# Optimization experiments

Hardware: AMD Instinct MI355X
Metric: run time of the kernel (lower is better)

## Reference

```python
import jax, jax.numpy as jnp
import numpy as np

EMBED_DIMS = 128
NUM_HEADS = 4
NUM_LAYERS = 3
OUT_CHANNELS = 20
PROJECT_SCALE = 4
VOXEL_SIZE = 0.2
SCENE_FULL = (256, 256, 32)
SCENE = tuple(s // PROJECT_SCALE for s in SCENE_FULL)  # (64, 64, 8)
NQ = SCENE[0] * SCENE[1] * SCENE[2]                    # 32768
N_INST = 100
NUM_CLS = 21
IMAGE_SHAPE = (48, 160)
ORI_IMAGE_SHAPE = (384, 1280)
SCORE_THR, MASK_THR, IOU_THR = 0.25, 0.5, 0.8
DILATIONS = (1, 2, 3)


def _generate_grid(grid_shape, value):
    axes = [np.linspace(0, v - 1, s, dtype=np.float32) for s, v in zip(grid_shape, value)]
    return np.stack(np.meshgrid(*axes, indexing='ij'), 0)


def _layer_norm(x, g, b):
    mu = x.mean(-1, keepdims=True)
    var = ((x - mu) ** 2).mean(-1, keepdims=True)
    return (x - mu) * jax.lax.rsqrt(var + 1e-5) * g + b


def _mha(q, k, v, bias, in_w, in_b, out_w, out_b):
    C = q.shape[-1]
    H, D = NUM_HEADS, q.shape[-1] // NUM_HEADS
    wq, wk, wv = jnp.split(in_w, 3, axis=0)
    bq, bk, bv = jnp.split(in_b, 3)
    qh = (q @ wq.T + bq).reshape(q.shape[0], q.shape[1], H, D)
    kh = (k @ wk.T + bk).reshape(k.shape[0], k.shape[1], H, D)
    vh = (v @ wv.T + bv).reshape(v.shape[0], v.shape[1], H, D)
    s = jnp.einsum('bqhd,bkhd->bhqk', qh, kh) * (1.0 / np.sqrt(D)) + bias
    a = jax.nn.softmax(s, axis=-1)
    o = jnp.einsum('bhqk,bkhd->bqhd', a, vh).reshape(q.shape)
    return o @ out_w.T + out_b


def _conv3d(x, w, b, dilation):
    pad = (w.shape[-1] // 2) * dilation
    y = jax.lax.conv_general_dilated(
        x, w, window_strides=(1, 1, 1), padding=[(pad, pad)] * 3,
        rhs_dilation=(dilation,) * 3,
        dimension_numbers=('NCDHW', 'OIDHW', 'NCDHW'))
    return y + b[None, :, None, None, None]


def _forward(inst_queries, pred_logits, pred_masks, depth, K, E, voxel_origin,
             query_embed_w, pos_embed_w, attn_in_w, attn_in_b, attn_out_w,
             attn_out_b, ln1_g, ln1_b, ffn_w1, ffn_b1, ffn_w2, ffn_b2,
             ln2_g, ln2_b, proc_w, proc_b, out_w, out_b, fov_mask):
    C = EMBED_DIMS
    h, w = IMAGE_SHAPE
    n = pred_masks.shape[1]
    # buffers (compile-time constants)
    image_grid = jnp.asarray(_generate_grid(IMAGE_SHAPE, ORI_IMAGE_SHAPE)[::-1].copy())  # [2,h,w] (x,y)
    qp = (_generate_grid(SCENE, SCENE) + 0.5) * VOXEL_SIZE * PROJECT_SCALE
    query_pos0 = jnp.asarray(qp.reshape(3, -1).T)[None]  # [1,NQ,3]

    # panoptic postprocess (masked form, bs=1; invalid instance slots masked, not dropped)
    probs = jax.nn.softmax(jax.nn.sigmoid(pred_logits) / 0.06, axis=-1)
    scores = probs.max(-1)[0]              # [n]; labels.ne(num_classes) always True
    keep0 = scores > SCORE_THR
    pm = jax.nn.sigmoid(pred_masks[0])     # [n,h,w]
    prob_masks = jnp.where(keep0[:, None, None], scores[:, None, None] * pm, -1.0)
    mask_ids = jnp.argmax(prob_masks, axis=0)   # [h,w]
    masks = (mask_ids[None] == jnp.arange(n)[:, None, None]) & keep0[:, None, None]
    mask_area = masks.reshape(n, -1).sum(-1).astype(jnp.float32)
    pm_bin = pm >= MASK_THR
    pm_area = pm_bin.reshape(n, -1).sum(-1).astype(jnp.float32)
    masks = masks & pm_bin
    inter = masks.reshape(n, -1).sum(-1)
    keep = keep0 & (inter > 0) & (mask_area >= IOU_THR * pm_area)
    masks = masks & keep[:, None, None]
    any_keep = keep.any()

    # gather_mask_pos: back-project masked pixels to 3D and sum per instance
    d = depth.reshape(1, 1, h, w)
    grid = jnp.concatenate([image_grid[None] * d, d], axis=1).reshape(1, 3, h * w)
    cam = jnp.linalg.inv(K) @ grid
    hom = jnp.concatenate([cam, jnp.ones((1, 1, h * w), cam.dtype)], axis=1)
    pts = (jnp.linalg.inv(E) @ hom)[0, :3].T       # [HW,3]
    inst_xyz = masks.reshape(n, -1).astype(pts.dtype) @ pts  # [n,3] gather-mask-sum
    inst_pos = (inst_xyz @ pos_embed_w.T)[None]    # [1,n,C]

    # cross-attention over all scene queries; fov gather/scatter folded into final where,
    # valid because per-query computation is independent in cross-attn + per-token FFN/LN.
    qpos = (query_pos0 + voxel_origin) @ pos_embed_w.T        # [1,NQ,C]
    use = jnp.where(any_keep, 1.0, 0.0).astype(inst_queries.dtype)
    kv_k = inst_queries + use * inst_pos
    key_mask = jnp.where(any_keep, keep, True)
    bias = jnp.where(key_mask, 0.0, -1e9)[None, None, None, :]  # [1,1,1,n]
    q = query_embed_w[None]
    for li in range(NUM_LAYERS):
        x = q + qpos
        a = _mha(x, kv_k, inst_queries, bias, attn_in_w[li], attn_in_b[li],
                 attn_out_w[li], attn_out_b[li])
        x = _layer_norm(a + x, ln1_g[li], ln1_b[li])
        f = jax.nn.gelu(x @ ffn_w1[li].T + ffn_b1[li], approximate=False) @ ffn_w2[li].T + ffn_b2[li]
        q = _layer_norm(f + x, ln2_g[li], ln2_b[li])

    q = jnp.where(fov_mask[..., None], q, query_embed_w[None])   # scatter-update query_embed_src[fov_mask]
    x3d = q.reshape(1, *SCENE, C).transpose(0, 4, 1, 2, 3)       # [1,C,X,Y,Z]
    for i, dil in enumerate(DILATIONS):                          # Process: dilated residual convs
        x3d = jax.nn.relu(_conv3d(x3d, proc_w[i], proc_b[i], dil) + x3d)
    return _conv3d(x3d, out_w, out_b, 1)                         # [1,out_ch,X,Y,Z]


def setup_inputs():
    key = jax.random.key(0)
    ks = jax.random.split(key, 16)
    C, L = EMBED_DIMS, NUM_LAYERS
    s = 0.02
    inp = {}
    inp['inst_queries'] = jax.random.normal(ks[0], (1, N_INST, C), jnp.float32)
    inp['pred_logits'] = jax.random.normal(ks[1], (1, N_INST, NUM_CLS), jnp.float32)
    inp['pred_masks'] = jax.random.normal(ks[2], (1, N_INST) + IMAGE_SHAPE, jnp.float32) * 2.0
    inp['depth'] = jax.random.uniform(ks[3], (1,) + IMAGE_SHAPE, jnp.float32, 1.0, 50.0)
    inp['K'] = jnp.array([[[500.0, 0.0, 640.0], [0.0, 500.0, 192.0], [0.0, 0.0, 1.0]]], jnp.float32)
    inp['E'] = jnp.eye(4, dtype=jnp.float32).at[:3, 3].set(jnp.array([0.5, -0.3, 1.2]))[None]
    inp['voxel_origin'] = jax.random.normal(ks[4], (1, 1, 3), jnp.float32)
    inp['query_embed_w'] = jax.random.normal(ks[5], (NQ, C), jnp.float32) * s
    inp['pos_embed_w'] = jax.random.normal(ks[6], (C, 3), jnp.float32) * 2e-4
    inp['attn_in_w'] = jax.random.normal(ks[7], (L, 3 * C, C), jnp.float32) * s
    inp['attn_in_b'] = jnp.zeros((L, 3 * C), jnp.float32)
    inp['attn_out_w'] = jax.random.normal(ks[8], (L, C, C), jnp.float32) * s
    inp['attn_out_b'] = jnp.zeros((L, C), jnp.float32)
    inp['ln1_g'] = jnp.ones((L, C), jnp.float32)
    inp['ln1_b'] = jnp.zeros((L, C), jnp.float32)
    inp['ffn_w1'] = jax.random.normal(ks[9], (L, 4 * C, C), jnp.float32) * s
    inp['ffn_b1'] = jnp.zeros((L, 4 * C), jnp.float32)
    inp['ffn_w2'] = jax.random.normal(ks[10], (L, C, 4 * C), jnp.float32) * s
    inp['ffn_b2'] = jnp.zeros((L, C), jnp.float32)
    inp['ln2_g'] = jnp.ones((L, C), jnp.float32)
    inp['ln2_b'] = jnp.zeros((L, C), jnp.float32)
    inp['proc_w'] = jax.random.normal(ks[11], (3, C, C, 3, 3, 3), jnp.float32) * s
    inp['proc_b'] = jnp.zeros((3, C), jnp.float32)
    inp['out_w'] = jax.random.normal(ks[12], (OUT_CHANNELS, C, 1, 1, 1), jnp.float32) * s
    inp['out_b'] = jnp.zeros((OUT_CHANNELS,), jnp.float32)
    inp['fov_mask'] = jax.random.bernoulli(ks[13], 0.5, (1, NQ))
    return inp


def reference(inst_queries, pred_logits, pred_masks, depth, K, E, voxel_origin,
              query_embed_w, pos_embed_w, attn_in_w, attn_in_b, attn_out_w,
              attn_out_b, ln1_g, ln1_b, ffn_w1, ffn_b1, ffn_w2, ffn_b2,
              ln2_g, ln2_b, proc_w, proc_b, out_w, out_b, fov_mask):
    return _forward(inst_queries, pred_logits, pred_masks, depth, K, E, voxel_origin,
                    query_embed_w, pos_embed_w, attn_in_w, attn_in_b, attn_out_w,
                    attn_out_b, ln1_g, ln1_b, ffn_w1, ffn_b1, ffn_w2, ffn_b2,
                    ln2_g, ln2_b, proc_w, proc_b, out_w, out_b, fov_mask)
```

## Files before the change

### kernel.cpp

```cpp
#include <hip/hip_runtime.h>
#include <math.h>

typedef unsigned short u16;
typedef unsigned int   u32;

#define NQv 32768
#define HWp 7680
#define NI  100

typedef short v8s __attribute__((ext_vector_type(8)));
typedef float v4f __attribute__((ext_vector_type(4)));

__device__ inline float bf2f(u16 u){ u32 x = ((u32)u) << 16; return __uint_as_float(x); }
__device__ inline u16 f2bf(float f){
  u32 x = __float_as_uint(f);
  u32 r = (x + 0x7fffu + ((x >> 16) & 1u)) >> 16;
  return (u16)r;
}
__device__ inline float sigf(float x){ return 1.0f / (1.0f + expf(-x)); }

typedef const __attribute__((address_space(1))) void* gas_t;
typedef __attribute__((address_space(3))) void* las_t;

__global__ void k_prep_small(const float* __restrict__ Km, const float* __restrict__ Em,
                             const float* __restrict__ logits,
                             float* __restrict__ mats, float* __restrict__ scores,
                             int* __restrict__ keep0)
{
  int tid = threadIdx.x;
  if (tid == 0) {
    double a[9];
    for (int i = 0; i < 9; i++) a[i] = (double)Km[i];
    double det = a[0]*(a[4]*a[8]-a[5]*a[7]) - a[1]*(a[3]*a[8]-a[5]*a[6]) + a[2]*(a[3]*a[7]-a[4]*a[6]);
    double id = 1.0 / det;
    double inv[9];
    inv[0]=(a[4]*a[8]-a[5]*a[7])*id; inv[1]=(a[2]*a[7]-a[1]*a[8])*id; inv[2]=(a[1]*a[5]-a[2]*a[4])*id;
    inv[3]=(a[5]*a[6]-a[3]*a[8])*id; inv[4]=(a[0]*a[8]-a[2]*a[6])*id; inv[5]=(a[2]*a[3]-a[0]*a[5])*id;
    inv[6]=(a[3]*a[7]-a[4]*a[6])*id; inv[7]=(a[1]*a[6]-a[0]*a[7])*id; inv[8]=(a[0]*a[4]-a[1]*a[3])*id;
    for (int i = 0; i < 9; i++) mats[i] = (float)inv[i];
    double m[4][8];
    for (int r = 0; r < 4; r++){
      for (int c = 0; c < 4; c++){ m[r][c] = (double)Em[r*4+c]; m[r][4+c] = (r==c) ? 1.0 : 0.0; }
    }
    for (int col = 0; col < 4; col++){
      int piv = col; double best = fabs(m[col][col]);
      for (int r = col+1; r < 4; r++){ double v = fabs(m[r][col]); if (v > best){ best = v; piv = r; } }
      if (piv != col){ for (int c = 0; c < 8; c++){ double t = m[col][c]; m[col][c] = m[piv][c]; m[piv][c] = t; } }
      double p = m[col][col];
      for (int c = 0; c < 8; c++) m[col][c] /= p;
      for (int r = 0; r < 4; r++) if (r != col){ double f = m[r][col]; for (int c = 0; c < 8; c++) m[r][c] -= f*m[col][c]; }
    }
    for (int r = 0; r < 3; r++) for (int c = 0; c < 4; c++) mats[9 + r*4 + c] = (float)m[r][4+c];
  }
  if (tid < NI) {
    float mx = -1e30f;
    for (int c = 0; c < 21; c++){ float t = sigf(logits[tid*21+c]) / 0.06f; mx = fmaxf(mx, t); }
    float s = 0.f;
    for (int c = 0; c < 21; c++){ float t = sigf(logits[tid*21+c]) / 0.06f; s += expf(t - mx); }
    float sc = 1.0f / s;
    scores[tid] = sc;
    keep0[tid] = (sc > 0.25f) ? 1 : 0;
  }
}

__global__ void k_prep_multi(
    const float* __restrict__ s0, u16* __restrict__ d0, int n0,
    const float* __restrict__ s1, u16* __restrict__ d1, int n1,
    const float* __restrict__ s2, u16* __restrict__ d2, int n2,
    const float* __restrict__ s3, u16* __restrict__ d3, int n3,
    u16* __restrict__ z0, int zn0, u16* __restrict__ z1, int zn1,
    u16* __restrict__ z2, int zn2,
    const float* __restrict__ pe, float* __restrict__ peT)
{
  int i = blockIdx.x*256 + threadIdx.x;
  if (i < n0){ d0[i] = f2bf(s0[i]); return; } i -= n0;
  if (i < n1){ d1[i] = f2bf(s1[i]); return; } i -= n1;
  if (i < n2){ d2[i] = f2bf(s2[i]); return; } i -= n2;
  if (i < n3){ d3[i] = f2bf(s3[i]); return; } i -= n3;
  if (i < zn0){ z0[i] = 0; return; } i -= zn0;
  if (i < zn1){ z1[i] = 0; return; } i -= zn1;
  if (i < zn2){ z2[i] = 0; return; } i -= zn2;
  if (i < 384){ int d = i >> 7, c = i & 127; peT[i] = pe[c*3 + d]; }
}

__global__ __launch_bounds__(256) void k_mask_argmax2(
    const float* __restrict__ pmL, const float* __restrict__ scores,
    const int* __restrict__ keep0, int* __restrict__ mids)
{
  __shared__ float sv[4][64];
  __shared__ int   si[4][64];
  int tid = threadIdx.x, lane = tid & 63, w = tid >> 6;
  int p = blockIdx.x*64 + lane;
  float best = -2e30f; int bid = 0;
  #pragma unroll 5
  for (int jj = 0; jj < 25; jj++){
    int i = w*25 + jj;
    float lg = pmL[i*HWp + p];
    float val = keep0[i] ? scores[i] * sigf(lg) : -1.0f;
    if (val > best){ best = val; bid = i; }
  }
  sv[w][lane] = best; si[w][lane] = bid;
  __syncthreads();
  if (w == 0){
    float b0 = sv[0][lane]; int i0 = si[0][lane];
    #pragma unroll
    for (int g = 1; g < 4; g++){
      float bg = sv[g][lane]; int ig = si[g][lane];
      if (bg > b0 || (bg == b0 && ig < i0)){ b0 = bg; i0 = ig; }
    }
    mids[p] = i0;
  }
}

__global__ __launch_bounds__(256) void k_instbp(
    const float* __restrict__ pmL, const int* __restrict__ mids,
    const int* __restrict__ keep0, const float* __restrict__ depth,
    const float* __restrict__ mats, int* __restrict__ keep, float* __restrict__ xyz)
{
  int i = blockIdx.x, tid = threadIdx.x;
  int k0 = keep0[i];
  int ma = 0, pa = 0, it = 0;
  for (int p = tid; p < HWp; p += 256){
    float lg = pmL[i*HWp + p];
    int pb = (lg >= 0.0f) ? 1 : 0;
    int mi = (mids[p] == i && k0) ? 1 : 0;
    ma += mi; pa += pb; it += (mi & pb);
  }
  __shared__ int sma[256], spa[256], sit[256];
  __shared__ int s_keep;
  sma[tid] = ma; spa[tid] = pa; sit[tid] = it;
  __syncthreads();
  for (int off = 128; off; off >>= 1){
    if (tid < off){ sma[tid]+=sma[tid+off]; spa[tid]+=spa[tid+off]; sit[tid]+=sit[tid+off]; }
    __syncthreads();
  }
  if (tid == 0){
    int kk = (k0 && sit[0] > 0 && ((float)sma[0] >= 0.8f*(float)spa[0])) ? 1 : 0;
    keep[i] = kk; s_keep = kk;
  }
  __syncthreads();
  float sx = 0.f, sy = 0.f, sz = 0.f;
  if (s_keep){
    float ik0=mats[0],ik1=mats[1],ik2=mats[2],ik3=mats[3],ik4=mats[4],ik5=mats[5],ik6=mats[6],ik7=mats[7],ik8=mats[8];
    const float* iE = mats + 9;
    for (int p = tid; p < HWp; p += 256){
      if (mids[p] == i && pmL[i*HWp + p] >= 0.0f){
        int r = p / 160, c = p % 160;
        float xg = (float)((double)c * (1279.0/159.0));
        float yg = (float)((double)r * (383.0/47.0));
        float d = depth[p];
        float g0 = xg*d, g1 = yg*d, g2 = d;
        float c0 = ik0*g0 + ik1*g1 + ik2*g2;
        float c1 = ik3*g0 + ik4*g1 + ik5*g2;
        float c2 = ik6*g0 + ik7*g1 + ik8*g2;
        sx += iE[0]*c0 + iE[1]*c1 + iE[2]*c2 + iE[3];
        sy += iE[4]*c0 + iE[5]*c1 + iE[6]*c2 + iE[7];
        sz += iE[8]*c0 + iE[9]*c1 + iE[10]*c2 + iE[11];
      }
    }
  }
  __shared__ float rx[256], ry[256], rz[256];
  rx[tid]=sx; ry[tid]=sy; rz[tid]=sz;
  __syncthreads();
  for (int off = 128; off; off >>= 1){
    if (tid < off){ rx[tid]+=rx[tid+off]; ry[tid]+=ry[tid+off]; rz[tid]+=rz[tid+off]; }
    __syncthreads();
  }
  if (tid == 0){ xyz[i*3+0]=rx[0]; xyz[i*3+1]=ry[0]; xyz[i*3+2]=rz[0]; }
}

__global__ void k_kvk(const float* __restrict__ iq, const float* __restrict__ pe,
                      const float* __restrict__ xyz, const int* __restrict__ keep,
                      float* __restrict__ kvk)
{
  int tid = threadIdx.x;
  unsigned long long b = __ballot(tid < 100 && keep[tid] != 0);
  __shared__ int s_w[4];
  if ((tid & 63) == 0) s_w[tid >> 6] = (b != 0ULL);
  __syncthreads();
  float u = (s_w[0] | s_w[1]) ? 1.0f : 0.0f;
  int idx = blockIdx.x*256 + tid;
  if (idx >= NI*128) return;
  int i = idx >> 7, c = idx & 127;
  float ip = pe[c*3+0]*xyz[i*3+0] + pe[c*3+1]*xyz[i*3+1] + pe[c*3+2]*xyz[i*3+2];
  kvk[idx] = iq[idx] + u * ip;
}

__global__ __launch_bounds__(512) void k_khvh2(const float* __restrict__ kvk,
    const float* __restrict__ iq, const float* __restrict__ Win,
    const float* __restrict__ bin, const int* __restrict__ keep,
    float* __restrict__ biasArr, u16* __restrict__ khs_bf, u16* __restrict__ vt_bf)
{
  __shared__ u16 s_in[NI][130];
  __shared__ u16 s_w[64][130];
  __shared__ int s_any[8];
  int li = blockIdx.x, c0 = blockIdx.y*64;
  bool isK = (c0 < 128);
  const float* srcIn = isK ? kvk : iq;
  int tid = threadIdx.x;
  unsigned long long bm = __ballot(tid < 100 && keep[tid] != 0);
  if ((tid & 63) == 0) s_any[tid >> 6] = (bm != 0ULL);
  for (int i = tid; i < NI*128; i += 512) s_in[i>>7][i&127] = f2bf(srcIn[i]);
  const float* wbase = Win + ((size_t)li*384 + 128 + c0)*128;
  for (int i = tid; i < 64*128; i += 512) s_w[i>>7][i&127] = f2bf(wbase[i]);
  __syncthreads();
  if (li == 0 && c0 == 0 && tid < 128){
    int any = s_any[0] | s_any[1];
    float bb;
    if (tid < NI) bb = any ? (keep[tid] ? 0.0f : -1e9f) : 0.0f;
    else bb = -1e9f;
    biasArr[tid] = bb;
  }
  for (int o = tid; o < NI*64; o += 512){
    int k = o >> 6, c = o & 63;
    float acc = 0.f;
    #pragma unroll 8
    for (int j = 0; j < 128; j++) acc += bf2f(s_in[k][j]) * bf2f(s_w[c][j]);
    int cc = c0 + c;
    float v = acc + bin[li*384 + 128 + cc];
    int ch = cc & 127;
    int h = ch >> 5, dim = ch & 31;
    size_t hb = ((size_t)li*4 + h)*4096;
    if (isK){
      int kt = k >> 4, c16 = k & 15, r4q = dim >> 3, d = dim & 7;
      khs_bf[hb + kt*512 + (r4q*16 + c16)*8 + d] = f2bf(v * 0.17677669529663687f);
    } else {
      int dt = dim >> 4, c16d = dim & 15, ks = k >> 5, r4k = (k >> 3) & 3, d = k & 7;
      vt_bf[hb + (ks*2 + dt)*512 + (r4k*16 + c16d)*8 + d] = f2bf(v);
    }
  }
}

__global__ __launch_bounds__(256) void k_packconv2(const float* __restrict__ w, u16* __restrict__ wp)
{
  __shared__ u16 s[3456];
  int o = blockIdx.x, li = blockIdx.y;
  const float* src = w + ((size_t)li*128 + o)*3456;
  for (int t = threadIdx.x; t < 3456; t += 256) s[t] = f2bf(src[t]);
  __syncthreads();
  for (int e = threadIdx.x; e < 3456; e += 256){
    int t = e >> 7, i = e & 127;
    wp[(((size_t)li*27 + t)*128 + o)*128 + i] = s[i*27 + t];
  }
}

__device__ inline void stage128(const u16* __restrict__ G, u16* lds,
                                int rbase, int pitchK, int kofs)
{
  int lane = threadIdx.x & 63, w = threadIdx.x >> 6;
  #pragma unroll
  for (int s = 0; s < 4; s++){
    int ldsOff = s*8192 + w*1024 + lane*16;
    int row = ldsOff >> 8;
    int cb  = ldsOff & 255;
    int scb = cb ^ ((row & 7) << 4);
    const u16* src = G + (size_t)(rbase + row)*pitchK + kofs + (scb >> 1);
    u16* dst = lds + (s*4096 + w*512);
    __builtin_amdgcn_global_load_lds((gas_t)src, (las_t)dst, 16, 0, 0);
  }
}

__device__ inline void copy32k(const u16* __restrict__ G, u16* lds)
{
  int lane = threadIdx.x & 63, w = threadIdx.x >> 6;
  #pragma unroll
  for (int s = 0; s < 4; s++){
    int off = s*4096 + w*512;
    const u16* src = G + off + lane*8;
    __builtin_amdgcn_global_load_lds((gas_t)src, (las_t)(lds + off), 16, 0, 0);
  }
}

__device__ inline void stageConvA4(const u16* __restrict__ X, const u16* __restrict__ zp,
                                   u16* lds, int m0, int dx, int dy)
{
  int lane = threadIdx.x & 63, w = threadIdx.x >> 6;
  #pragma unroll
  for (int s = 0; s < 4; s++){
    int ldsOff = s*8192 + w*1024 + lane*16;
    int row = ldsOff >> 8;
    int cb  = ldsOff & 255;
    int scb = cb ^ ((row & 7) << 4);
    int sidx = m0 + row;
    int xs = (sidx >> 9) + dx, ys = ((sidx >> 3) & 63) + dy, zs = sidx & 7;
    bool ok = ((unsigned)xs < 64u) & ((unsigned)ys < 64u);
    const u16* src = ok ? (X + (size_t)((xs*64+ys)*8+zs)*128 + (scb>>1)) : (zp + (scb>>1));
    u16* dst = lds + (s*4096 + w*512);
    __builtin_amdgcn_global_load_lds((gas_t)src, (las_t)dst, 16, 0, 0);
  }
}

__device__ inline v8s fragld(const u16* base, int row, int cb){
  return *(const v8s*)(base + row*128 + (((cb) ^ ((row & 7) << 4)) >> 1));
}

__device__ inline void compute128(const u16* As, const u16* Bs,
                                  int wm, int wn, int r15, int kg, v4f acc[2][4])
{
  #pragma unroll
  for (int k0 = 0; k0 < 4; k0++){
    int cb = k0*64 + kg*16;
    v8s a0 = fragld(As, wm*32 +      r15, cb);
    v8s a1 = fragld(As, wm*32 + 16 + r15, cb);
    v8s b0 = fragld(Bs, wn*64 +      r15, cb);
    v8s b1 = fragld(Bs, wn*64 + 16 + r15, cb);
    v8s b2 = fragld(Bs, wn*64 + 32 + r15, cb);
    v8s b3 = fragld(Bs, wn*64 + 48 + r15, cb);
    acc[0][0] = __builtin_amdgcn_mfma_f32_16x16x32_bf16(a0, b0, acc[0][0], 0, 0, 0);
    acc[0][1] = __builtin_amdgcn_mfma_f32_16x16x32_bf16(a0, b1, acc[0][1], 0, 0, 0);
    acc[0][2] = __builtin_amdgcn_mfma_f32_16x16x32_bf16(a0, b2, acc[0][2], 0, 0, 0);
    acc[0][3] = __builtin_amdgcn_mfma_f32_16x16x32_bf16(a0, b3, acc[0][3], 0, 0, 0);
    acc[1][0] = __builtin_amdgcn_mfma_f32_16x16x32_bf16(a1, b0, acc[1][0], 0, 0, 0);
    acc[1][1] = __builtin_amdgcn_mfma_f32_16x16x32_bf16(a1, b1, acc[1][1], 0, 0, 0);
    acc[1][2] = __builtin_amdgcn_mfma_f32_16x16x32_bf16(a1, b2, acc[1][2], 0, 0, 0);
    acc[1][3] = __builtin_amdgcn_mfma_f32_16x16x32_bf16(a1, b3, acc[1][3], 0, 0, 0);
  }
}

__global__ __launch_bounds__(512) void k_layer(
    const void* __restrict__ srcv, int srcBf,
    const float* __restrict__ peT, const float* __restrict__ vo,
    const u16* __restrict__ ainQ, const float* __restrict__ ainQb,
    const u16* __restrict__ khs, const u16* __restrict__ vt,
    const float* __restrict__ biasArr,
    const u16* __restrict__ aoutw, const float* __restrict__ aoutb,
    const float* __restrict__ g1, const float* __restrict__ b1v,
    const u16* __restrict__ w1p, const float* __restrict__ b1p,
    const u16* __restrict__ w2p, const float* __restrict__ b2p,
    const float* __restrict__ g2, const float* __restrict__ b2v,
    u16* __restrict__ outB, const int* __restrict__ fov, const float* __restrict__ qe)
{
  extern __shared__ u16 smem[];
  u16* SA = smem;
  u16* SB = smem + 16384;
  u16* X  = smem + 32768;
  u16* Rh = smem + 49152;
  char* Xc = (char*)X;
  char* Rc = (char*)Rh;
  int tid = threadIdx.x, lane = tid & 63, w = tid >> 6;
  int wm = w & 3, wn = w >> 2, r15 = lane & 15, kg = lane >> 4;
  int m0 = blockIdx.x * 128;

  stage128(ainQ, SA, 0, 128, 0);
  copy32k(khs, Rh);
  copy32k(vt, Rh + 16384);
  {
    int r = tid >> 2, c0 = (tid & 3)*32;
    int q = m0 + r;
    float px = ((float)(q >> 9)       + 0.5f)*0.8f + vo[0];
    float py = ((float)((q >> 3)&63)  + 0.5f)*0.8f + vo[1];
    float pz = ((float)(q & 7)        + 0.5f)*0.8f + vo[2];
    char* arow = Xc + r*256;
    int rx = (r & 7) << 4;
    if (!srcBf){
      const float4* sp  = (const float4*)((const float*)srcv + (size_t)q*128 + c0);
      const float4* pex = (const float4*)(peT +   0 + c0);
      const float4* pey = (const float4*)(peT + 128 + c0);
      const float4* pez = (const float4*)(peT + 256 + c0);
      #pragma unroll
      for (int j = 0; j < 8; j++){
        float4 v = sp[j];
        float4 ax = pex[j], ay = pey[j], az = pez[j];
        float o0 = v.x + ax.x*px + ay.x*py + az.x*pz;
        float o1 = v.y + ax.y*px + ay.y*py + az.y*pz;
        float o2 = v.z + ax.z*px + ay.z*py + az.z*pz;
        float o3 = v.w + ax.w*px + ay.w*py + az.w*pz;
        int cbyte = (c0 + j*4)*2;
        *(u32*)(arow + ((cbyte    ) ^ rx)) = (u32)f2bf(o0) | ((u32)f2bf(o1) << 16);
        *(u32*)(arow + ((cbyte + 4) ^ rx)) = (u32)f2bf(o2) | ((u32)f2bf(o3) << 16);
      }
    } else {
      const u16* sp = (const u16*)srcv + (size_t)q*128 + c0;
      #pragma unroll
      for (int j = 0; j < 4; j++){
        v8s t = *(const v8s*)(sp + j*8);
        #pragma unroll
        for (int pr = 0; pr < 4; pr++){
          int c = c0 + j*8 + pr*2;
          float e0 = bf2f((u16)t[pr*2])   + peT[c]*px   + peT[128+c]*py   + peT[256+c]*pz;
          float e1 = bf2f((u16)t[pr*2+1]) + peT[c+1]*px + peT[128+c+1]*py + peT[256+c+1]*pz;
          *(u32*)(arow + ((c*2) ^ rx)) = (u32)f2bf(e0) | ((u32)f2bf(e1) << 16);
        }
      }
    }
  }
  __syncthreads();

  {
    v4f acc[2][4] = {};
    compute128(X, SA, wm, wn, r15, kg, acc);
    #pragma unroll
    for (int i = 0; i < 2; i++){
      #pragma unroll
      for (int j = 0; j < 4; j++){
        int col = wn*64 + j*16 + r15;
        float bv = ainQb[col];
        #pragma unroll
        for (int rr = 0; rr < 4; rr++){
          int row = wm*32 + i*16 + kg*4 + rr;
          *(u16*)((char*)SB + row*256 + (((col*2)) ^ ((row & 7) << 4))) = f2bf(acc[i][j][rr] + bv);
        }
      }
    }
  }
  __syncthreads();

  {
    int c = lane & 15, r4 = lane >> 4;
    char* pwc = (char*)(SA + w*2048);
    int qrow_base = w*16;
    #pragma unroll
    for (int h = 0; h < 4; h++){
      const u16* Kh = Rh + h*4096;
      const u16* Vh = Rh + 16384 + h*4096;
      int qrow = qrow_base + c;
      v8s qf = *(const v8s*)((char*)SB + qrow*256 + ((h*64 + r4*16) ^ ((qrow & 7) << 4)));
      v4f s[8] = {{0,0,0,0},{0,0,0,0},{0,0,0,0},{0,0,0,0},{0,0,0,0},{0,0,0,0},{0,0,0,0},{0,0,0,0}};
      #pragma unroll
      for (int kt = 0; kt < 8; kt++){
        v8s kf = *(const v8s*)(Kh + kt*512 + lane*8);
        s[kt] = __builtin_amdgcn_mfma_f32_16x16x32_bf16(kf, qf, s[kt], 0, 0, 0);
      }
      float mx = -1e30f;
      #pragma unroll
      for (int kt = 0; kt < 8; kt++){
        float4 bb = *(const float4*)(biasArr + kt*16 + r4*4);
        s[kt][0] += bb.x; s[kt][1] += bb.y; s[kt][2] += bb.z; s[kt][3] += bb.w;
        mx = fmaxf(mx, fmaxf(fmaxf(s[kt][0], s[kt][1]), fmaxf(s[kt][2], s[kt][3])));
      }
      mx = fmaxf(mx, __shfl_xor(mx, 16, 64));
      mx = fmaxf(mx, __shfl_xor(mx, 32, 64));
      float sum = 0.f;
      #pragma unroll
      for (int kt = 0; kt < 8; kt++){
        #pragma unroll
        for (int rg = 0; rg < 4; rg++){
          float p = __expf(s[kt][rg] - mx);
          s[kt][rg] = p; sum += p;
        }
      }
      sum += __shfl_xor(sum, 16, 64);
      sum += __shfl_xor(sum, 32, 64);
      float inv = 1.0f / sum;
      int rxq = (c & 7) << 4;
      #pragma unroll
      for (int kt = 0; kt < 8; kt++){
        #pragma unroll
        for (int pr = 0; pr < 2; pr++){
          u32 pk = (u32)f2bf(s[kt][pr*2]*inv) | ((u32)f2bf(s[kt][pr*2+1]*inv) << 16);
          int colb = kt*32 + r4*8 + pr*4;
          *(u32*)(pwc + c*256 + (colb ^ rxq)) = pk;
        }
      }
      v4f o[2] = {{0,0,0,0},{0,0,0,0}};
      #pragma unroll
      for (int ks = 0; ks < 4; ks++){
        v8s aP = *(const v8s*)(pwc + c*256 + ((ks*64 + r4*16) ^ rxq));
        #pragma unroll
        for (int dt = 0; dt < 2; dt++){
          v8s vf = *(const v8s*)(Vh + (ks*2 + dt)*512 + lane*8);
          o[dt] = __builtin_amdgcn_mfma_f32_16x16x32_bf16(aP, vf, o[dt], 0, 0, 0);
        }
      }
      #pragma unroll
      for (int dt = 0; dt < 2; dt++){
        #pragma unroll
        for (int rg = 0; rg < 4; rg++){
          int row = qrow_base + r4*4 + rg;
          int col = h*32 + dt*16 + c;
          *(u16*)((char*)SB + row*256 + ((col*2) ^ ((row & 7) << 4))) = f2bf(o[dt][rg]);
        }
      }
    }
  }
  __syncthreads();

  stage128(aoutw, SA, 0, 128, 0);
  __syncthreads();
  {
    v4f acc[2][4] = {};
    compute128(SB, SA, wm, wn, r15, kg, acc);
    #pragma unroll
    for (int i = 0; i < 2; i++){
      #pragma unroll
      for (int j = 0; j < 4; j++){
        int col = wn*64 + j*16 + r15;
        float bv = aoutb[col];
        #pragma unroll
        for (int rr = 0; rr < 4; rr++){
          int row = wm*32 + i*16 + kg*4 + rr;
          float xres = bf2f(*(const u16*)(Xc + row*256 + ((col*2) ^ ((row & 7) << 4))));
          float y = acc[i][j][rr] + bv + xres;
          *(float*)(Rc + row*512 + ((col*4) ^ ((row & 7) << 4))) = y;
        }
      }
    }
  }
  __syncthreads();

  {
    int r = tid >> 2, j4 = tid & 3;
    float vals[32];
    int rx = (r & 7) << 4;
    #pragma unroll
    for (int k = 0; k < 32; k++){
      int c = j4 + 4*k;
      vals[k] = *(const float*)(Rc + r*512 + ((c*4) ^ rx));
    }
    float s = 0.f;
    #pragma unroll
    for (int k = 0; k < 32; k++) s += vals[k];
    s += __shfl_xor(s, 1, 64); s += __shfl_xor(s, 2, 64);
    float mean = s * (1.0f/128.0f);
    float vv = 0.f;
    #pragma unroll
    for (int k = 0; k < 32; k++){ float d = vals[k] - mean; vv += d*d; }
    vv += __shfl_xor(vv, 1, 64); vv += __shfl_xor(vv, 2, 64);
    float rs = rsqrtf(vv*(1.0f/128.0f) + 1e-5f);
    #pragma unroll
    for (int k = 0; k < 32; k++){
      int c = j4 + 4*k;
      float o = (vals[k] - mean)*rs*g1[c] + b1v[c];
      *(float*)(Rc + r*512 + ((c*4) ^ rx)) = o;
      *(u16*)(Xc + r*256 + ((c*2) ^ rx)) = f2bf(o);
    }
  }
  __syncthreads();

  v4f acc2[2][4] = {};
  for (int nt = 0; nt < 4; nt++){
    stage128(w1p, SA, nt*128, 128, 0);
    stage128(w2p, SB, 0, 512, nt*128);
    __syncthreads();
    v4f a1[2][4] = {};
    compute128(X, SA, wm, wn, r15, kg, a1);
    __syncthreads();
    #pragma unroll
    for (int i = 0; i < 2; i++){
      #pragma unroll
      for (int j = 0; j < 4; j++){
        int col = wn*64 + j*16 + r15;
        float bv = b1p[nt*128 + col];
        #pragma unroll
        for (int rr = 0; rr < 4; rr++){
          int row = wm*32 + i*16 + kg*4 + rr;
          float hv = a1[i][j][rr] + bv;
          float u2 = hv*(0.7978845608028654f + 0.0356774081f*hv*hv);
          hv = hv / (1.0f + __expf(-2.0f*u2));
          *(u16*)((char*)SA + row*256 + ((col*2) ^ ((row & 7) << 4))) = f2bf(hv);
        }
      }
    }
    __syncthreads();
    compute128(SA, SB, wm, wn, r15, kg, acc2);
    __syncthreads();
  }

  {
    #pragma unroll
    for (int i = 0; i < 2; i++){
      #pragma unroll
      for (int j = 0; j < 4; j++){
        int col = wn*64 + j*16 + r15;
        float bv = b2p[col];
        #pragma unroll
        for (int rr = 0; rr < 4; rr++){
          int row = wm*32 + i*16 + kg*4 + rr;
          char* p = Rc + row*512 + ((col*4) ^ ((row & 7) << 4));
          float y = acc2[i][j][rr] + bv + *(const float*)p;
          *(float*)p = y;
        }
      }
    }
  }
  __syncthreads();

  {
    int r = tid >> 2, j4 = tid & 3;
    float vals[32];
    int rx = (r & 7) << 4;
    #pragma unroll
    for (int k = 0; k < 32; k++){
      int c = j4 + 4*k;
      vals[k] = *(const float*)(Rc + r*512 + ((c*4) ^ rx));
    }
    float s = 0.f;
    #pragma unroll
    for (int k = 0; k < 32; k++) s += vals[k];
    s += __shfl_xor(s, 1, 64); s += __shfl_xor(s, 2, 64);
    float mean = s * (1.0f/128.0f);
    float vv = 0.f;
    #pragma unroll
    for (int k = 0; k < 32; k++){ float d = vals[k] - mean; vv += d*d; }
    vv += __shfl_xor(vv, 1, 64); vv += __shfl_xor(vv, 2, 64);
    float rs = rsqrtf(vv*(1.0f/128.0f) + 1e-5f);
    int gq = m0 + r;
    #pragma unroll
    for (int k = 0; k < 32; k++){
      int c = j4 + 4*k;
      float o = (vals[k] - mean)*rs*g2[c] + b2v[c];
      if (fov){
        outB[(size_t)gq*128 + c] = f2bf(fov[gq] ? o : qe[(size_t)gq*128 + c]);
      } else {
        outB[(size_t)gq*128 + c] = f2bf(o);
      }
    }
  }
}

__global__ __launch_bounds__(512) void k_conv4(
    const u16* __restrict__ X, const u16* __restrict__ W,
    const float* __restrict__ bias, const u16* __restrict__ zp,
    u16* __restrict__ Y, int dil)
{
  extern __shared__ u16 smem[];
  u16* bufA0 = smem;
  u16* bufA1 = smem + 16384;
  u16* bufW0 = smem + 32768;
  u16* bufW1 = smem + 49152;
  int tid = threadIdx.x, lane = tid & 63, w = tid >> 6;
  int wk = w & 1, wm = (w >> 1) & 1, wn = (w >> 2) & 1;
  int r15 = lane & 15, kg = lane >> 4;
  int bid = blockIdx.x;
  int lb = (bid & 7)*32 + (bid >> 3);
  int m0 = lb*128;
  v4f acc[4][4] = {};
  const v8s vzero = {0,0,0,0,0,0,0,0};
  stageConvA4(X, zp, bufA0, m0, -dil, -dil);
  stage128(W, bufW0, 0, 128, 0);
  for (int g = 0; g < 9; g++){
    const u16* As = (g & 1) ? bufA1 : bufA0;
    #pragma unroll
    for (int dzi = 0; dzi < 3; dzi++){
      int t = g*3 + dzi;
      const u16* Ws = (t & 1) ? bufW1 : bufW0;
      if (t + 1 < 27)
        stage128(W + (size_t)(t+1)*16384, ((t+1)&1) ? bufW1 : bufW0, 0, 128, 0);
      if (dzi == 0 && g < 8){
        int gn = g + 1;
        stageConvA4(X, zp, (gn & 1) ? bufA1 : bufA0, m0, (gn/3 - 1)*dil, (gn%3 - 1)*dil);
      }
      if (dzi == 0){
        if (g < 8) asm volatile("s_waitcnt vmcnt(8)" ::: "memory");
        else       asm volatile("s_waitcnt vmcnt(4)" ::: "memory");
      } else {
        if (t < 26) asm volatile("s_waitcnt vmcnt(4)" ::: "memory");
        else        asm volatile("s_waitcnt vmcnt(0)" ::: "memory");
      }
      __builtin_amdgcn_s_barrier();
      asm volatile("" ::: "memory");
      int zofs = (dzi - 1)*dil;
      bool okz = (unsigned)((r15 & 7) + zofs) < 8u;
      #pragma unroll
      for (int k0 = 0; k0 < 2; k0++){
        int cb = wk*128 + k0*64 + kg*16;
        v8s a[4], b[4];
        #pragma unroll
        for (int q = 0; q < 4; q++){
          int ra = wm*64 + q*16 + r15 + zofs;
          int rc = min(max(ra, 0), 127);
          a[q] = okz ? fragld(As, rc, cb) : vzero;
          b[q] = fragld(Ws, wn*64 + q*16 + r15, cb);
        }
        #pragma unroll
        for (int i = 0; i < 4; i++)
          #pragma unroll
          for (int j = 0; j < 4; j++)
            acc[i][j] = __builtin_amdgcn_mfma_f32_16x16x32_bf16(a[i], b[j], acc[i][j], 0, 0, 0);
      }
      asm volatile("" ::: "memory");
      __builtin_amdgcn_s_barrier();
      asm volatile("" ::: "memory");
    }
  }
  float* red = (float*)smem;
  if (wk == 0){
    #pragma unroll
    for (int i = 0; i < 4; i++)
      #pragma unroll
      for (int j = 0; j < 4; j++)
        #pragma unroll
        for (int rr = 0; rr < 4; rr++)
          red[(wm*64 + i*16 + kg*4 + rr)*128 + wn*64 + j*16 + r15] = acc[i][j][rr];
  }
  __syncthreads();
  if (wk == 1){
    #pragma unroll
    for (int i = 0; i < 4; i++){
      #pragma unroll
      for (int j = 0; j < 4; j++){
        int col = wn*64 + j*16 + r15;
        float bv = bias[col];
        #pragma unroll
        for (int rr = 0; rr < 4; rr++){
          int row = wm*64 + i*16 + kg*4 + rr;
          int grow = m0 + row;
          float v = acc[i][j][rr] + red[row*128 + col] + bv + bf2f(X[(size_t)grow*128 + col]);
          v = fmaxf(v, 0.0f);
          Y[(size_t)grow*128 + col] = f2bf(v);
        }
      }
    }
  }
}

__global__ __launch_bounds__(256) void k_outconv(const u16* __restrict__ X,
    const float* __restrict__ W, const float* __restrict__ B, float* __restrict__ out)
{
  __shared__ float sw[20*128];
  __shared__ float sbb[20];
  int tid = threadIdx.x;
  for (int i = tid; i < 20*128; i += 256) sw[i] = W[i];
  if (tid < 20) sbb[tid] = B[tid];
  __syncthreads();
  int s = blockIdx.x*256 + tid;
  u32 rv[64];
  const u32* xp = (const u32*)(X + (size_t)s*128);
  #pragma unroll
  for (int j = 0; j < 64; j++) rv[j] = xp[j];
  for (int ot = 0; ot < 20; ot++){
    float acc = sbb[ot];
    #pragma unroll
    for (int j = 0; j < 64; j++){
      u32 u = rv[j];
      acc += bf2f((u16)(u & 0xffff))*sw[ot*128 + 2*j] + bf2f((u16)(u >> 16))*sw[ot*128 + 2*j + 1];
    }
    out[(size_t)ot*NQv + s] = acc;
  }
}

extern "C" void kernel_launch(void* const* d_in, const int* in_sizes, int n_in,
                              void* d_out, int out_size, void* d_ws, size_t ws_size,
                              hipStream_t stream)
{
  const float* iq    = (const float*)d_in[0];
  const float* logits= (const float*)d_in[1];
  const float* pmL   = (const float*)d_in[2];
  const float* depth = (const float*)d_in[3];
  const float* Km    = (const float*)d_in[4];
  const float* Em    = (const float*)d_in[5];
  const float* vo    = (const float*)d_in[6];
  const float* qe    = (const float*)d_in[7];
  const float* pe    = (const float*)d_in[8];
  const float* ain_w = (const float*)d_in[9];
  const float* ain_b = (const float*)d_in[10];
  const float* aout_w= (const float*)d_in[11];
  const float* aout_b= (const float*)d_in[12];
  const float* ln1g  = (const float*)d_in[13];
  const float* ln1b  = (const float*)d_in[14];
  const float* w1    = (const float*)d_in[15];
  const float* b1    = (const float*)d_in[16];
  const float* w2    = (const float*)d_in[17];
  const float* b2    = (const float*)d_in[18];
  const float* ln2g  = (const float*)d_in[19];
  const float* ln2b  = (const float*)d_in[20];
  const float* pw    = (const float*)d_in[21];
  const float* pb    = (const float*)d_in[22];
  const float* ow    = (const float*)d_in[23];
  const float* ob    = (const float*)d_in[24];
  const int*   fov   = (const int*)d_in[25];
  float* out = (float*)d_out;

  (void)hipFuncSetAttribute((const void*)k_layer, hipFuncAttributeMaxDynamicSharedMemorySize, 163840);
  (void)hipFuncSetAttribute((const void*)k_conv4, hipFuncAttributeMaxDynamicSharedMemorySize, 131072);

  char* ws = (char*)d_ws;
  size_t off = 0;
  auto alloc = [&](size_t bytes) -> char* {
    char* p = ws + off;
    off = (off + bytes + 255) & ~(size_t)255;
    return p;
  };
  float* mats    = (float*)alloc(32*4);
  float* scores  = (float*)alloc(128*4);
  int*   keep0   = (int*)  alloc(128*4);
  int*   keep    = (int*)  alloc(128*4);
  float* biasArr = (float*)alloc(128*4);
  float* xyz     = (float*)alloc(512*4);
  u16*   zp      = (u16*)  alloc(256);
  float* peT     = (float*)alloc(384*4);
  int*   mids    = (int*)  alloc((size_t)HWp*4);
  float* kvkb    = (float*)alloc((size_t)NI*128*4);
  u16* khs_bf  = (u16*)alloc((size_t)3*4*128*32*2);
  u16* vt_bf   = (u16*)alloc((size_t)3*4*32*128*2);
  u16* ain_bf  = (u16*)alloc((size_t)3*384*128*2);
  u16* aout_bf = (u16*)alloc((size_t)3*128*128*2);
  u16* w1_bf   = (u16*)alloc((size_t)3*512*128*2);
  u16* w2_bf   = (u16*)alloc((size_t)3*128*512*2);
  u16* wc_bf   = (u16*)alloc((size_t)3*27*128*128*2);
  u16* T2bf = (u16*)alloc((size_t)NQv*128*2);
  u16* x3a  = (u16*)alloc((size_t)NQv*128*2);
  u16* x3b  = (u16*)alloc((size_t)NQv*128*2);
  (void)ws_size; (void)in_sizes; (void)n_in; (void)out_size;

  k_prep_small<<<1,128,0,stream>>>(Km, Em, logits, mats, scores, keep0);
  {
    int n0 = 3*384*128, n1 = 3*128*128, n2 = 3*512*128, n3 = 3*128*512;
    int zn0 = 3*4*128*32, zn1 = 3*4*32*128, zn2 = 128;
    int total = n0+n1+n2+n3+zn0+zn1+zn2+384;
    k_prep_multi<<<(total+255)/256,256,0,stream>>>(
        ain_w, ain_bf, n0, aout_w, aout_bf, n1, w1, w1_bf, n2, w2, w2_bf, n3,
        khs_bf, zn0, vt_bf, zn1, zp, zn2, pe, peT);
  }
  k_packconv2<<<dim3(128,3),256,0,stream>>>(pw, wc_bf);
  k_mask_argmax2<<<120,256,0,stream>>>(pmL, scores, keep0, mids);
  k_instbp<<<NI,256,0,stream>>>(pmL, mids, keep0, depth, mats, keep, xyz);
  k_kvk<<<(NI*128+255)/256,256,0,stream>>>(iq, pe, xyz, keep, kvkb);
  { dim3 g(3,4); k_khvh2<<<g,512,0,stream>>>(kvkb, iq, ain_w, ain_b, keep, biasArr, khs_bf, vt_bf); }

  for (int li = 0; li < 3; li++){
    const void* src = (li == 0) ? (const void*)qe : (const void*)T2bf;
    u16* outT = (li < 2) ? T2bf : x3a;
    k_layer<<<256,512,163840,stream>>>(
        src, (li == 0) ? 0 : 1, peT, vo,
        ain_bf + (size_t)li*384*128, ain_b + li*384,
        khs_bf + (size_t)li*16384, vt_bf + (size_t)li*16384, biasArr,
        aout_bf + (size_t)li*128*128, aout_b + li*128,
        ln1g + li*128, ln1b + li*128,
        w1_bf + (size_t)li*512*128, b1 + li*512,
        w2_bf + (size_t)li*128*512, b2 + li*128,
        ln2g + li*128, ln2b + li*128,
        outT, (li == 2) ? fov : nullptr, qe);
  }

  k_conv4<<<256,512,131072,stream>>>(x3a, wc_bf + (size_t)0*27*16384, pb + 0,   zp, x3b, 1);
  k_conv4<<<256,512,131072,stream>>>(x3b, wc_bf + (size_t)1*27*16384, pb + 128, zp, x3a, 2);
  k_conv4<<<256,512,131072,stream>>>(x3a, wc_bf + (size_t)2*27*16384, pb + 256, zp, x3b, 3);
  k_outconv<<<128,256,0,stream>>>(x3b, ow, ob, out);
}
```

Measured before the change: 362.3 us.

## Halve k_layer tile to 64 queries and shrink LDS to fit more blocks

Restructures the fused transformer layer kernel to process 64 query rows per block instead of 128, doubling the grid to 512 blocks. LDS use drops from 160KB to 80KB by reusing three 32KB-class buffers, loading K/V heads in two halves, and keeping residuals in bf16 rather than fp32. The aim is more concurrent blocks per CU and better use of all CUs on the GPU. In exchange it adds extra barriers, restages weight tiles twice as often across blocks, and rounds the FFN residual to bf16, which may change numerics slightly.

```diff
diff --git a/kernel.cpp b/kernel.cpp
--- a/kernel.cpp
+++ b/kernel.cpp
@@ -260,11 +260,11 @@
   }
 }
 
-__device__ inline void copy32k(const u16* __restrict__ G, u16* lds)
+__device__ inline void copy16k(const u16* __restrict__ G, u16* lds)
 {
   int lane = threadIdx.x & 63, w = threadIdx.x >> 6;
   #pragma unroll
-  for (int s = 0; s < 4; s++){
+  for (int s = 0; s < 2; s++){
     int off = s*4096 + w*512;
     const u16* src = G + off + lane*8;
     __builtin_amdgcn_global_load_lds((gas_t)src, (las_t)(lds + off), 16, 0, 0);
@@ -294,30 +294,24 @@
   return *(const v8s*)(base + row*128 + (((cb) ^ ((row & 7) << 4)) >> 1));
 }
 
-__device__ inline void compute128(const u16* As, const u16* Bs,
-                                  int wm, int wn, int r15, int kg, v4f acc[2][4])
+__device__ inline void compute64(const u16* As, const u16* Bs,
+                                 int wm, int wn, int r15, int kg, v4f acc[2][2])
 {
   #pragma unroll
   for (int k0 = 0; k0 < 4; k0++){
     int cb = k0*64 + kg*16;
     v8s a0 = fragld(As, wm*32 +      r15, cb);
     v8s a1 = fragld(As, wm*32 + 16 + r15, cb);
-    v8s b0 = fragld(Bs, wn*64 +      r15, cb);
-    v8s b1 = fragld(Bs, wn*64 + 16 + r15, cb);
-    v8s b2 = fragld(Bs, wn*64 + 32 + r15, cb);
-    v8s b3 = fragld(Bs, wn*64 + 48 + r15, cb);
+    v8s b0 = fragld(Bs, wn*32 +      r15, cb);
+    v8s b1 = fragld(Bs, wn*32 + 16 + r15, cb);
     acc[0][0] = __builtin_amdgcn_mfma_f32_16x16x32_bf16(a0, b0, acc[0][0], 0, 0, 0);
     acc[0][1] = __builtin_amdgcn_mfma_f32_16x16x32_bf16(a0, b1, acc[0][1], 0, 0, 0);
-    acc[0][2] = __builtin_amdgcn_mfma_f32_16x16x32_bf16(a0, b2, acc[0][2], 0, 0, 0);
-    acc[0][3] = __builtin_amdgcn_mfma_f32_16x16x32_bf16(a0, b3, acc[0][3], 0, 0, 0);
     acc[1][0] = __builtin_amdgcn_mfma_f32_16x16x32_bf16(a1, b0, acc[1][0], 0, 0, 0);
     acc[1][1] = __builtin_amdgcn_mfma_f32_16x16x32_bf16(a1, b1, acc[1][1], 0, 0, 0);
-    acc[1][2] = __builtin_amdgcn_mfma_f32_16x16x32_bf16(a1, b2, acc[1][2], 0, 0, 0);
-    acc[1][3] = __builtin_amdgcn_mfma_f32_16x16x32_bf16(a1, b3, acc[1][3], 0, 0, 0);
-  }
-}
-
-__global__ __launch_bounds__(512) void k_layer(
+  }
+}
+
+__global__ __launch_bounds__(512, 4) void k_layer(
     const void* __restrict__ srcv, int srcBf,
     const float* __restrict__ peT, const float* __restrict__ vo,
     const u16* __restrict__ ainQ, const float* __restrict__ ainQb,
@@ -331,48 +325,43 @@
     u16* __restrict__ outB, const int* __restrict__ fov, const float* __restrict__ qe)
 {
   extern __shared__ u16 smem[];
-  u16* SA = smem;
-  u16* SB = smem + 16384;
-  u16* X  = smem + 32768;
-  u16* Rh = smem + 49152;
-  char* Xc = (char*)X;
-  char* Rc = (char*)Rh;
+  u16* A = smem;
+  u16* B = smem + 16384;
+  u16* C = smem + 32768;
+  char* Ac = (char*)A;
+  char* Cc = (char*)C;
   int tid = threadIdx.x, lane = tid & 63, w = tid >> 6;
-  int wm = w & 3, wn = w >> 2, r15 = lane & 15, kg = lane >> 4;
-  int m0 = blockIdx.x * 128;
-
-  stage128(ainQ, SA, 0, 128, 0);
-  copy32k(khs, Rh);
-  copy32k(vt, Rh + 16384);
+  int wm = w & 1, wn = w >> 1, r15 = lane & 15, kg = lane >> 4;
+  int m0 = blockIdx.x * 64;
+
+  stage128(ainQ, A, 0, 128, 0);
+  copy16k(khs, B);
+  copy16k(vt, B + 8192);
   {
-    int r = tid >> 2, c0 = (tid & 3)*32;
+    int r = tid >> 3, c0 = (tid & 7)*16;
     int q = m0 + r;
     float px = ((float)(q >> 9)       + 0.5f)*0.8f + vo[0];
     float py = ((float)((q >> 3)&63)  + 0.5f)*0.8f + vo[1];
     float pz = ((float)(q & 7)        + 0.5f)*0.8f + vo[2];
-    char* arow = Xc + r*256;
+    char* arow = Cc + r*256;
     int rx = (r & 7) << 4;
     if (!srcBf){
       const float4* sp  = (const float4*)((const float*)srcv + (size_t)q*128 + c0);
-      const float4* pex = (const float4*)(peT +   0 + c0);
-      const float4* pey = (const float4*)(peT + 128 + c0);
-      const float4* pez = (const float4*)(peT + 256 + c0);
-      #pragma unroll
-      for (int j = 0; j < 8; j++){
+      #pragma unroll
+      for (int j = 0; j < 4; j++){
         float4 v = sp[j];
-        float4 ax = pex[j], ay = pey[j], az = pez[j];
-        float o0 = v.x + ax.x*px + ay.x*py + az.x*pz;
-        float o1 = v.y + ax.y*px + ay.y*py + az.y*pz;
-        float o2 = v.z + ax.z*px + ay.z*py + az.z*pz;
-        float o3 = v.w + ax.w*px + ay.w*py + az.w*pz;
-        int cbyte = (c0 + j*4)*2;
-        *(u32*)(arow + ((cbyte    ) ^ rx)) = (u32)f2bf(o0) | ((u32)f2bf(o1) << 16);
-        *(u32*)(arow + ((cbyte + 4) ^ rx)) = (u32)f2bf(o2) | ((u32)f2bf(o3) << 16);
+        int c = c0 + j*4;
+        float o0 = v.x + peT[c]*px   + peT[128+c]*py   + peT[256+c]*pz;
+        float o1 = v.y + peT[c+1]*px + peT[128+c+1]*py + peT[256+c+1]*pz;
+        float o2 = v.z + peT[c+2]*px + peT[128+c+2]*py + peT[256+c+2]*pz;
+        float o3 = v.w + peT[c+3]*px + peT[128+c+3]*py + peT[256+c+3]*pz;
+        *(u32*)(arow + ((c*2    ) ^ rx)) = (u32)f2bf(o0) | ((u32)f2bf(o1) << 16);
+        *(u32*)(arow + ((c*2 + 4) ^ rx)) = (u32)f2bf(o2) | ((u32)f2bf(o3) << 16);
       }
     } else {
       const u16* sp = (const u16*)srcv + (size_t)q*128 + c0;
       #pragma unroll
-      for (int j = 0; j < 4; j++){
+      for (int j = 0; j < 2; j++){
         v8s t = *(const v8s*)(sp + j*8);
         #pragma unroll
         for (int pr = 0; pr < 4; pr++){
@@ -387,18 +376,19 @@
   __syncthreads();
 
   {
-    v4f acc[2][4] = {};
-    compute128(X, SA, wm, wn, r15, kg, acc);
+    v4f acc[2][2] = {};
+    compute64(C, A, wm, wn, r15, kg, acc);
+    __syncthreads();
     #pragma unroll
     for (int i = 0; i < 2; i++){
       #pragma unroll
-      for (int j = 0; j < 4; j++){
-        int col = wn*64 + j*16 + r15;
+      for (int j = 0; j < 2; j++){
+        int col = wn*32 + j*16 + r15;
         float bv = ainQb[col];
         #pragma unroll
         for (int rr = 0; rr < 4; rr++){
           int row = wm*32 + i*16 + kg*4 + rr;
-          *(u16*)((char*)SB + row*256 + (((col*2)) ^ ((row & 7) << 4))) = f2bf(acc[i][j][rr] + bv);
+          *(u16*)(Ac + row*256 + ((col*2) ^ ((row & 7) << 4))) = f2bf(acc[i][j][rr] + bv);
         }
       }
     }
@@ -407,19 +397,32 @@
 
   {
     int c = lane & 15, r4 = lane >> 4;
-    char* pwc = (char*)(SA + w*2048);
-    int qrow_base = w*16;
-    #pragma unroll
-    for (int h = 0; h < 4; h++){
-      const u16* Kh = Rh + h*4096;
-      const u16* Vh = Rh + 16384 + h*4096;
-      int qrow = qrow_base + c;
-      v8s qf = *(const v8s*)((char*)SB + qrow*256 + ((h*64 + r4*16) ^ ((qrow & 7) << 4)));
+    int qt = w & 3, hsel = w >> 2;
+    int qrow = qt*16 + c;
+    v8s qf[2];
+    #pragma unroll
+    for (int p = 0; p < 2; p++){
+      int h = p*2 + hsel;
+      qf[p] = *(const v8s*)(Ac + qrow*256 + ((h*64 + r4*16) ^ ((qrow & 7) << 4)));
+    }
+    __syncthreads();
+    char* pwc = (char*)(A + w*2048);
+    v4f out[2][2];
+    #pragma unroll
+    for (int p = 0; p < 2; p++){
+      if (p == 1){
+        __syncthreads();
+        copy16k(khs + 8192, B);
+        copy16k(vt + 8192, B + 8192);
+        __syncthreads();
+      }
+      const u16* Kh = B + hsel*4096;
+      const u16* Vh = B + 8192 + hsel*4096;
       v4f s[8] = {{0,0,0,0},{0,0,0,0},{0,0,0,0},{0,0,0,0},{0,0,0,0},{0,0,0,0},{0,0,0,0},{0,0,0,0}};
       #pragma unroll
       for (int kt = 0; kt < 8; kt++){
         v8s kf = *(const v8s*)(Kh + kt*512 + lane*8);
-        s[kt] = __builtin_amdgcn_mfma_f32_16x16x32_bf16(kf, qf, s[kt], 0, 0, 0);
+        s[kt] = __builtin_amdgcn_mfma_f32_16x16x32_bf16(kf, qf[p], s[kt], 0, 0, 0);
       }
       float mx = -1e30f;
       #pragma unroll
@@ -435,8 +438,8 @@
       for (int kt = 0; kt < 8; kt++){
         #pragma unroll
         for (int rg = 0; rg < 4; rg++){
-          float p = __expf(s[kt][rg] - mx);
-          s[kt][rg] = p; sum += p;
+          float pp = __expf(s[kt][rg] - mx);
+          s[kt][rg] = pp; sum += pp;
         }
       }
       sum += __shfl_xor(sum, 16, 64);
@@ -452,46 +455,64 @@
           *(u32*)(pwc + c*256 + (colb ^ rxq)) = pk;
         }
       }
-      v4f o[2] = {{0,0,0,0},{0,0,0,0}};
+      out[p][0] = (v4f){0,0,0,0}; out[p][1] = (v4f){0,0,0,0};
       #pragma unroll
       for (int ks = 0; ks < 4; ks++){
         v8s aP = *(const v8s*)(pwc + c*256 + ((ks*64 + r4*16) ^ rxq));
         #pragma unroll
         for (int dt = 0; dt < 2; dt++){
           v8s vf = *(const v8s*)(Vh + (ks*2 + dt)*512 + lane*8);
-          o[dt] = __builtin_amdgcn_mfma_f32_16x16x32_bf16(aP, vf, o[dt], 0, 0, 0);
-        }
-      }
+          out[p][dt] = __builtin_amdgcn_mfma_f32_16x16x32_bf16(aP, vf, out[p][dt], 0, 0, 0);
+        }
+      }
+    }
+    __syncthreads();
+    #pragma unroll
+    for (int p = 0; p < 2; p++){
+      int h = p*2 + hsel;
       #pragma unroll
       for (int dt = 0; dt < 2; dt++){
         #pragma unroll
         for (int rg = 0; rg < 4; rg++){
-          int row = qrow_base + r4*4 + rg;
+          int row = qt*16 + r4*4 + rg;
           int col = h*32 + dt*16 + c;
-          *(u16*)((char*)SB + row*256 + ((col*2) ^ ((row & 7) << 4))) = f2bf(o[dt][rg]);
-        }
-      }
-    }
-  }
-  __syncthreads();
-
-  stage128(aoutw, SA, 0, 128, 0);
+          *(u16*)((char*)B + row*256 + ((col*2) ^ ((row & 7) << 4))) = f2bf(out[p][dt][rg]);
+        }
+      }
+    }
+  }
+  __syncthreads();
+
+  stage128(aoutw, A, 0, 128, 0);
   __syncthreads();
   {
-    v4f acc[2][4] = {};
-    compute128(SB, SA, wm, wn, r15, kg, acc);
+    v4f acc[2][2] = {};
+    compute64(B, A, wm, wn, r15, kg, acc);
+    float yv[2][2][4];
     #pragma unroll
     for (int i = 0; i < 2; i++){
       #pragma unroll
-      for (int j = 0; j < 4; j++){
-        int col = wn*64 + j*16 + r15;
+      for (int j = 0; j < 2; j++){
+        int col = wn*32 + j*16 + r15;
         float bv = aoutb[col];
         #pragma unroll
         for (int rr = 0; rr < 4; rr++){
           int row = wm*32 + i*16 + kg*4 + rr;
-          float xres = bf2f(*(const u16*)(Xc + row*256 + ((col*2) ^ ((row & 7) << 4))));
-          float y = acc[i][j][rr] + bv + xres;
-          *(float*)(Rc + row*512 + ((col*4) ^ ((row & 7) << 4))) = y;
+          float xres = bf2f(*(const u16*)(Cc + row*256 + ((col*2) ^ ((row & 7) << 4))));
+          yv[i][j][rr] = acc[i][j][rr] + bv + xres;
+        }
+      }
+    }
+    __syncthreads();
+    #pragma unroll
+    for (int i = 0; i < 2; i++){
+      #pragma unroll
+      for (int j = 0; j < 2; j++){
+        int col = wn*32 + j*16 + r15;
+        #pragma unroll
+        for (int rr = 0; rr < 4; rr++){
+          int row = wm*32 + i*16 + kg*4 + rr;
+          *(float*)(Ac + row*512 + ((col*4) ^ ((row & 7) << 4))) = yv[i][j][rr];
         }
       }
     }
@@ -499,47 +520,46 @@
   __syncthreads();
 
   {
-    int r = tid >> 2, j4 = tid & 3;
-    float vals[32];
+    int r = tid >> 3, j8 = tid & 7;
+    float vals[16];
     int rx = (r & 7) << 4;
     #pragma unroll
-    for (int k = 0; k < 32; k++){
-      int c = j4 + 4*k;
-      vals[k] = *(const float*)(Rc + r*512 + ((c*4) ^ rx));
+    for (int k = 0; k < 16; k++){
+      int c = j8 + 8*k;
+      vals[k] = *(const float*)(Ac + r*512 + ((c*4) ^ rx));
     }
     float s = 0.f;
     #pragma unroll
-    for (int k = 0; k < 32; k++) s += vals[k];
-    s += __shfl_xor(s, 1, 64); s += __shfl_xor(s, 2, 64);
+    for (int k = 0; k < 16; k++) s += vals[k];
+    s += __shfl_xor(s, 1, 64); s += __shfl_xor(s, 2, 64); s += __shfl_xor(s, 4, 64);
     float mean = s * (1.0f/128.0f);
     float vv = 0.f;
     #pragma unroll
-    for (int k = 0; k < 32; k++){ float d = vals[k] - mean; vv += d*d; }
-    vv += __shfl_xor(vv, 1, 64); vv += __shfl_xor(vv, 2, 64);
+    for (int k = 0; k < 16; k++){ float d = vals[k] - mean; vv += d*d; }
+    vv += __shfl_xor(vv, 1, 64); vv += __shfl_xor(vv, 2, 64); vv += __shfl_xor(vv, 4, 64);
     float rs = rsqrtf(vv*(1.0f/128.0f) + 1e-5f);
     #pragma unroll
-    for (int k = 0; k < 32; k++){
-      int c = j4 + 4*k;
+    for (int k = 0; k < 16; k++){
+      int c = j8 + 8*k;
       float o = (vals[k] - mean)*rs*g1[c] + b1v[c];
-      *(float*)(Rc + r*512 + ((c*4) ^ rx)) = o;
-      *(u16*)(Xc + r*256 + ((c*2) ^ rx)) = f2bf(o);
-    }
-  }
-  __syncthreads();
-
-  v4f acc2[2][4] = {};
+      *(u16*)(Cc + r*256 + ((c*2) ^ rx)) = f2bf(o);
+    }
+  }
+  __syncthreads();
+
+  v4f acc2[2][2] = {};
   for (int nt = 0; nt < 4; nt++){
-    stage128(w1p, SA, nt*128, 128, 0);
-    stage128(w2p, SB, 0, 512, nt*128);
-    __syncthreads();
-    v4f a1[2][4] = {};
-    compute128(X, SA, wm, wn, r15, kg, a1);
+    stage128(w1p, A, nt*128, 128, 0);
+    stage128(w2p, B, 0, 512, nt*128);
+    __syncthreads();
+    v4f a1[2][2] = {};
+    compute64(C, A, wm, wn, r15, kg, a1);
     __syncthreads();
     #pragma unroll
     for (int i = 0; i < 2; i++){
       #pragma unroll
-      for (int j = 0; j < 4; j++){
-        int col = wn*64 + j*16 + r15;
+      for (int j = 0; j < 2; j++){
+        int col = wn*32 + j*16 + r15;
         float bv = b1p[nt*128 + col];
         #pragma unroll
         for (int rr = 0; rr < 4; rr++){
@@ -547,28 +567,40 @@
           float hv = a1[i][j][rr] + bv;
           float u2 = hv*(0.7978845608028654f + 0.0356774081f*hv*hv);
           hv = hv / (1.0f + __expf(-2.0f*u2));
-          *(u16*)((char*)SA + row*256 + ((col*2) ^ ((row & 7) << 4))) = f2bf(hv);
-        }
-      }
-    }
-    __syncthreads();
-    compute128(SA, SB, wm, wn, r15, kg, acc2);
+          *(u16*)(Ac + row*256 + ((col*2) ^ ((row & 7) << 4))) = f2bf(hv);
+        }
+      }
+    }
+    __syncthreads();
+    compute64(A, B, wm, wn, r15, kg, acc2);
     __syncthreads();
   }
 
   {
+    float yv[2][2][4];
     #pragma unroll
     for (int i = 0; i < 2; i++){
       #pragma unroll
-      for (int j = 0; j < 4; j++){
-        int col = wn*64 + j*16 + r15;
+      for (int j = 0; j < 2; j++){
+        int col = wn*32 + j*16 + r15;
         float bv = b2p[col];
         #pragma unroll
         for (int rr = 0; rr < 4; rr++){
           int row = wm*32 + i*16 + kg*4 + rr;
-          char* p = Rc + row*512 + ((col*4) ^ ((row & 7) << 4));
-          float y = acc2[i][j][rr] + bv + *(const float*)p;
-          *(float*)p = y;
+          float xres = bf2f(*(const u16*)(Cc + row*256 + ((col*2) ^ ((row & 7) << 4))));
+          yv[i][j][rr] = acc2[i][j][rr] + bv + xres;
+        }
+      }
+    }
+    #pragma unroll
+    for (int i = 0; i < 2; i++){
+      #pragma unroll
+      for (int j = 0; j < 2; j++){
+        int col = wn*32 + j*16 + r15;
+        #pragma unroll
+        for (int rr = 0; rr < 4; rr++){
+          int row = wm*32 + i*16 + kg*4 + rr;
+          *(float*)(Ac + row*512 + ((col*4) ^ ((row & 7) << 4))) = yv[i][j][rr];
         }
       }
     }
@@ -576,28 +608,28 @@
   __syncthreads();
 
   {
-    int r = tid >> 2, j4 = tid & 3;
-    float vals[32];
+    int r = tid >> 3, j8 = tid & 7;
+    float vals[16];
     int rx = (r & 7) << 4;
     #pragma unroll
-    for (int k = 0; k < 32; k++){
-      int c = j4 + 4*k;
-      vals[k] = *(const float*)(Rc + r*512 + ((c*4) ^ rx));
+    for (int k = 0; k < 16; k++){
+      int c = j8 + 8*k;
+      vals[k] = *(const float*)(Ac + r*512 + ((c*4) ^ rx));
     }
     float s = 0.f;
     #pragma unroll
-    for (int k = 0; k < 32; k++) s += vals[k];
-    s += __shfl_xor(s, 1, 64); s += __shfl_xor(s, 2, 64);
+    for (int k = 0; k < 16; k++) s += vals[k];
+    s += __shfl_xor(s, 1, 64); s += __shfl_xor(s, 2, 64); s += __shfl_xor(s, 4, 64);
     float mean = s * (1.0f/128.0f);
     float vv = 0.f;
     #pragma unroll
-    for (int k = 0; k < 32; k++){ float d = vals[k] - mean; vv += d*d; }
-    vv += __shfl_xor(vv, 1, 64); vv += __shfl_xor(vv, 2, 64);
+    for (int k = 0; k < 16; k++){ float d = vals[k] - mean; vv += d*d; }
+    vv += __shfl_xor(vv, 1, 64); vv += __shfl_xor(vv, 2, 64); vv += __shfl_xor(vv, 4, 64);
     float rs = rsqrtf(vv*(1.0f/128.0f) + 1e-5f);
     int gq = m0 + r;
     #pragma unroll
-    for (int k = 0; k < 32; k++){
-      int c = j4 + 4*k;
+    for (int k = 0; k < 16; k++){
+      int c = j8 + 8*k;
       float o = (vals[k] - mean)*rs*g2[c] + b2v[c];
       if (fov){
         outB[(size_t)gq*128 + c] = f2bf(fov[gq] ? o : qe[(size_t)gq*128 + c]);
@@ -761,7 +793,7 @@
   const int*   fov   = (const int*)d_in[25];
   float* out = (float*)d_out;
 
-  (void)hipFuncSetAttribute((const void*)k_layer, hipFuncAttributeMaxDynamicSharedMemorySize, 163840);
+  (void)hipFuncSetAttribute((const void*)k_layer, hipFuncAttributeMaxDynamicSharedMemorySize, 81920);
   (void)hipFuncSetAttribute((const void*)k_conv4, hipFuncAttributeMaxDynamicSharedMemorySize, 131072);
 
   char* ws = (char*)d_ws;
@@ -811,7 +843,7 @@
   for (int li = 0; li < 3; li++){
     const void* src = (li == 0) ? (const void*)qe : (const void*)T2bf;
     u16* outT = (li < 2) ? T2bf : x3a;
-    k_layer<<<256,512,163840,stream>>>(
+    k_layer<<<512,512,81920,stream>>>(
         src, (li == 0) ? 0 : 1, peT, vo,
         ain_bf + (size_t)li*384*128, ain_b + li*384,
         khs_bf + (size_t)li*16384, vt_bf + (size_t)li*16384, biasArr,
```

Measured after the change: 376.3 us. 1.04x slower.
